# Optimization experiments

Measured on AMD Instinct MI355X. Metric: run time of the kernel, lower is better.

The kernel has to match this reference:

```python
import jax, jax.numpy as jnp
import numpy as np

T, D, H, O = 16384, 512, 1024, 512


def setup_inputs() -> dict:
    key = jax.random.key(0)
    k_in, k_h0, kU, kW, kV = jax.random.split(key, 5)
    inputs = jax.random.randint(k_in, (T,), 0, D)
    h0 = jax.random.normal(k_h0, (H,), dtype=jnp.float32)
    U = jax.random.normal(kU, (H, D), dtype=jnp.float32) * 0.01
    W = jax.random.normal(kW, (H, H), dtype=jnp.float32) * 0.01
    V = jax.random.normal(kV, (O, H), dtype=jnp.float32) * 0.01
    bh = jnp.zeros((H,), dtype=jnp.float32)
    by = jnp.zeros((O,), dtype=jnp.float32)
    return {"inputs": inputs, "h0": h0, "U": U, "W": W, "V": V, "bh": bh, "by": by}


def reference(inputs, h0, U, W, V, bh, by):
    # U @ one_hot(x_t) is just a column gather of U; precompute for all t: (T, H)
    Ux = U.T[inputs]

    def step(h, ux):
        h = jnp.tanh(ux + W @ h + bh)  # (H,)
        return h, h

    h_T, hs = jax.lax.scan(step, h0, Ux)  # hs: (T, H)
    logits = hs @ V.T + by  # (T, O)
    return logits, h_T
```

## Files before the change

### kernel.cpp

```cpp
#include <hip/hip_runtime.h>
#include <cstdint>


constexpr int T_STEPS = 16384;
constexpr int D_DIM   = 512;
constexpr int H_DIM   = 1024;
constexpr int O_DIM   = 512;
constexpr int NBLK    = 32;
constexpr int NTHR    = 512;

__device__ __forceinline__ float fast_tanh(float x) {
    float e = __expf(2.f * x);
    return 1.f - 2.f / (e + 1.f);
}

__device__ __forceinline__ float hsum4(const float4& v) {
    return (v.x + v.y) + (v.z + v.w);
}

__global__ __launch_bounds__(NTHR, 2)
void rnn_fused(const int* __restrict__ xs, const float* __restrict__ h0,
               const float* __restrict__ U, const float* __restrict__ W,
               const float* __restrict__ V, const float* __restrict__ bh,
               const float* __restrict__ by, float* __restrict__ out,
               unsigned long long* __restrict__ htag)
{
    const int b   = blockIdx.x;
    const int tid = threadIdx.x;
    const int w   = tid >> 6;
    const int l   = tid & 63;

    __shared__ float hl[2][H_DIM];

    const int wr0 = b * 32 + w * 4;
    float4 wreg[4][4];
#pragma unroll
    for (int j = 0; j < 4; ++j)
#pragma unroll
        for (int q = 0; q < 4; ++q)
            wreg[j][q] = *(const float4*)(W + (size_t)(wr0 + j) * H_DIM + 16 * l + 4 * q);
    const float bh_r = bh[wr0 + (l & 3)];
    const int   urow = wr0 + (l & 3);

    const int vr0 = b * 16 + w * 2;
    float4 vreg[2][4];
#pragma unroll
    for (int m = 0; m < 2; ++m)
#pragma unroll
        for (int q = 0; q < 4; ++q)
            vreg[m][q] = *(const float4*)(V + (size_t)(vr0 + m) * H_DIM + 16 * l + 4 * q);
    const float by_r = by[vr0 + (l & 1)];

    int rdw[4];
#pragma unroll
    for (int q = 0; q < 4; ++q)
        rdw[q] = 16 * l + 4 * (q ^ ((l >> 1) & 3));
    const int c   = tid >> 3;
    const int qw  = (tid >> 1) & 3;
    const int wdw = 16 * c + 4 * (qw ^ ((c >> 1) & 3)) + 2 * (tid & 1);

    const bool o1 = (l & 1) != 0, o2 = (l & 2) != 0;

    for (int t = 0; t < T_STEPS; ++t) {
        const int sb = (~t) & 1;
        float* hb = hl[sb];

        const int   xt = xs[t];
        const float uv = U[(size_t)urow * D_DIM + xt];

        float2 hpair;
        if (t == 0) {
            hpair = *(const float2*)(h0 + 2 * tid);
        } else {
            const unsigned want = (unsigned)(t - 1);
            const unsigned long long* pp = htag + (size_t)((t - 1) & 1) * H_DIM + 2 * tid;
            unsigned long long q0, q1;
            do {
                q0 = __hip_atomic_load(pp + 0, __ATOMIC_RELAXED, __HIP_MEMORY_SCOPE_AGENT);
                q1 = __hip_atomic_load(pp + 1, __ATOMIC_RELAXED, __HIP_MEMORY_SCOPE_AGENT);
            } while ((unsigned)(q0 >> 32) != want || (unsigned)(q1 >> 32) != want);
            hpair = make_float2(__uint_as_float((unsigned)q0),
                                __uint_as_float((unsigned)q1));
        }
        *(float2*)&hb[wdw] = hpair;
        __syncthreads();

        float4 h4[4];
#pragma unroll
        for (int q = 0; q < 4; ++q) h4[q] = *(const float4*)&hb[rdw[q]];

        float s[4];
#pragma unroll
        for (int j = 0; j < 4; ++j) {
            float4 a = make_float4(0.f, 0.f, 0.f, 0.f);
#pragma unroll
            for (int q = 0; q < 4; ++q) {
                a.x += wreg[j][q].x * h4[q].x;
                a.y += wreg[j][q].y * h4[q].y;
                a.z += wreg[j][q].z * h4[q].z;
                a.w += wreg[j][q].w * h4[q].w;
            }
            s[j] = hsum4(a);
        }
        float A  = o1 ? s[1] : s[0], Ax = o1 ? s[0] : s[1];
        float B  = o1 ? s[3] : s[2], Bx = o1 ? s[2] : s[3];
        A += __shfl_xor(Ax, 1);
        B += __shfl_xor(Bx, 1);
        float Cv = o2 ? B : A, Cx = o2 ? A : B;
        Cv += __shfl_xor(Cx, 2);
        Cv += __shfl_xor(Cv, 4);
        Cv += __shfl_xor(Cv, 8);
        Cv += __shfl_xor(Cv, 16);
        Cv += __shfl_xor(Cv, 32);

        const float hv = fast_tanh(Cv + bh_r + uv);
        if (l < 4) {
            const unsigned long long pk =
                ((unsigned long long)(unsigned)t << 32) | (unsigned long long)__float_as_uint(hv);
            __hip_atomic_store(htag + (size_t)(t & 1) * H_DIM + wr0 + l, pk,
                               __ATOMIC_RELAXED, __HIP_MEMORY_SCOPE_AGENT);
        }

        if (t > 0) {
            float sv[2];
#pragma unroll
            for (int m = 0; m < 2; ++m) {
                float4 a = make_float4(0.f, 0.f, 0.f, 0.f);
#pragma unroll
                for (int q = 0; q < 4; ++q) {
                    a.x += vreg[m][q].x * h4[q].x;
                    a.y += vreg[m][q].y * h4[q].y;
                    a.z += vreg[m][q].z * h4[q].z;
                    a.w += vreg[m][q].w * h4[q].w;
                }
                sv[m] = hsum4(a);
            }
            float P  = o1 ? sv[1] : sv[0], Px = o1 ? sv[0] : sv[1];
            P += __shfl_xor(Px, 1);
            P += __shfl_xor(P, 2);
            P += __shfl_xor(P, 4);
            P += __shfl_xor(P, 8);
            P += __shfl_xor(P, 16);
            P += __shfl_xor(P, 32);
            if (l < 2) out[(size_t)(t - 1) * O_DIM + vr0 + l] = P + by_r;
        }
    }

    {
        const unsigned want = (unsigned)(T_STEPS - 1);
        const unsigned long long* pp = htag + (size_t)((T_STEPS - 1) & 1) * H_DIM + 2 * tid;
        unsigned long long q0, q1;
        do {
            q0 = __hip_atomic_load(pp + 0, __ATOMIC_RELAXED, __HIP_MEMORY_SCOPE_AGENT);
            q1 = __hip_atomic_load(pp + 1, __ATOMIC_RELAXED, __HIP_MEMORY_SCOPE_AGENT);
        } while ((unsigned)(q0 >> 32) != want || (unsigned)(q1 >> 32) != want);
        float2 hpair = make_float2(__uint_as_float((unsigned)q0),
                                   __uint_as_float((unsigned)q1));
        if (b == 0)
            *(float2*)&out[(size_t)T_STEPS * O_DIM + 2 * tid] = hpair;

        float* hb = hl[1];
        *(float2*)&hb[wdw] = hpair;
        __syncthreads();
        float4 h4[4];
#pragma unroll
        for (int q = 0; q < 4; ++q) h4[q] = *(const float4*)&hb[rdw[q]];
        float sv[2];
#pragma unroll
        for (int m = 0; m < 2; ++m) {
            float4 a = make_float4(0.f, 0.f, 0.f, 0.f);
#pragma unroll
            for (int q = 0; q < 4; ++q) {
                a.x += vreg[m][q].x * h4[q].x;
                a.y += vreg[m][q].y * h4[q].y;
                a.z += vreg[m][q].z * h4[q].z;
                a.w += vreg[m][q].w * h4[q].w;
            }
            sv[m] = hsum4(a);
        }
        float P  = o1 ? sv[1] : sv[0], Px = o1 ? sv[0] : sv[1];
        P += __shfl_xor(Px, 1);
        P += __shfl_xor(P, 2);
        P += __shfl_xor(P, 4);
        P += __shfl_xor(P, 8);
        P += __shfl_xor(P, 16);
        P += __shfl_xor(P, 32);
        if (l < 2) out[(size_t)(T_STEPS - 1) * O_DIM + vr0 + l] = P + by_r;
    }
}

extern "C" void kernel_launch(void* const* d_in, const int* in_sizes, int n_in,
                              void* d_out, int out_size, void* d_ws, size_t ws_size,
                              hipStream_t stream) {
    const int*   xs = (const int*)d_in[0];
    const float* h0 = (const float*)d_in[1];
    const float* U  = (const float*)d_in[2];
    const float* W  = (const float*)d_in[3];
    const float* V  = (const float*)d_in[4];
    const float* bh = (const float*)d_in[5];
    const float* by = (const float*)d_in[6];
    float* out = (float*)d_out;

    unsigned long long* htag = (unsigned long long*)d_ws;
    hipMemsetAsync(d_ws, 0xAA, 2 * H_DIM * sizeof(unsigned long long), stream);

    rnn_fused<<<NBLK, NTHR, 0, stream>>>(xs, h0, U, W, V, bh, by, out, htag);
}
```

Measured before the change: 22.87 ms.

## Co-locate all worker blocks on one XCD and poll a fast non-atomic tag copy

The kernel now launches 256 blocks. Each block reads its XCC_ID and registers in a per-XCD counter, and the first XCD to gather 32 blocks is elected; all other blocks exit. The intent is to keep the per-step cross-block handoff of h inside one XCD's L2 rather than crossing the fabric between dies. Hidden state is published twice, to a volatile copy and an agent-scope atomic copy, and consumers mostly poll the volatile copy, falling back to the atomic one every eighth try. This relies on hardware-specific co-residency and cache behaviour, risks deadlock if fewer than 32 blocks land on any one XCD, and the volatile reads may still see stale L2 data.

```diff
diff --git a/kernel.cpp b/kernel.cpp
--- a/kernel.cpp
+++ b/kernel.cpp
@@ -6,16 +6,43 @@
 constexpr int D_DIM   = 512;
 constexpr int H_DIM   = 1024;
 constexpr int O_DIM   = 512;
-constexpr int NBLK    = 32;
+constexpr int NGRID   = 256;
+constexpr int NWORK   = 32;
 constexpr int NTHR    = 512;
 
 __device__ __forceinline__ float fast_tanh(float x) {
     float e = __expf(2.f * x);
     return 1.f - 2.f / (e + 1.f);
 }
-
 __device__ __forceinline__ float hsum4(const float4& v) {
     return (v.x + v.y) + (v.z + v.w);
+}
+
+__device__ __forceinline__ float2 acquire_pair(
+    const volatile unsigned long long* fp,
+    const unsigned long long* sp, unsigned want)
+{
+    unsigned long long a, b;
+    int k = 0;
+    for (;;) {
+        if ((k++ & 7) != 7) {
+            a = fp[0];
+            b = fp[1];
+        } else {
+            a = __hip_atomic_load(sp + 0, __ATOMIC_RELAXED, __HIP_MEMORY_SCOPE_AGENT);
+            b = __hip_atomic_load(sp + 1, __ATOMIC_RELAXED, __HIP_MEMORY_SCOPE_AGENT);
+        }
+        if ((unsigned)(a >> 32) == want && (unsigned)(b >> 32) == want) break;
+    }
+    return make_float2(__uint_as_float((unsigned)a), __uint_as_float((unsigned)b));
+}
+
+__device__ __forceinline__ void publish(volatile unsigned long long* Fd,
+                                        unsigned long long* Sd,
+                                        unsigned long long pk)
+{
+    *Fd = pk;
+    __hip_atomic_store(Sd, pk, __ATOMIC_RELAXED, __HIP_MEMORY_SCOPE_AGENT);
 }
 
 __global__ __launch_bounds__(NTHR, 2)
@@ -23,12 +50,36 @@
                const float* __restrict__ U, const float* __restrict__ W,
                const float* __restrict__ V, const float* __restrict__ bh,
                const float* __restrict__ by, float* __restrict__ out,
-               unsigned long long* __restrict__ htag)
+               int* __restrict__ ctrl,
+               unsigned long long* __restrict__ htagF,
+               unsigned long long* __restrict__ htagS)
 {
-    const int b   = blockIdx.x;
     const int tid = threadIdx.x;
-    const int w   = tid >> 6;
-    const int l   = tid & 63;
+
+    __shared__ int s_slice;
+    if (tid == 0) {
+        int xcd;
+        asm volatile("s_getreg_b32 %0, hwreg(HW_REG_XCC_ID)" : "=s"(xcd));
+        xcd &= 7;
+        const int r = __hip_atomic_fetch_add(&ctrl[1 + xcd], 1,
+                                             __ATOMIC_RELAXED, __HIP_MEMORY_SCOPE_AGENT);
+        if (r == NWORK - 1) {
+            int expected = 0;
+            __hip_atomic_compare_exchange_strong(&ctrl[0], &expected, xcd + 1,
+                __ATOMIC_RELAXED, __ATOMIC_RELAXED, __HIP_MEMORY_SCOPE_AGENT);
+        }
+        int ch;
+        do {
+            ch = __hip_atomic_load(&ctrl[0], __ATOMIC_RELAXED, __HIP_MEMORY_SCOPE_AGENT);
+        } while (ch == 0);
+        s_slice = (ch - 1 == xcd && r < NWORK) ? r : -1;
+    }
+    __syncthreads();
+    const int b = s_slice;
+    if (b < 0) return;
+
+    const int w = tid >> 6;
+    const int l = tid & 63;
 
     __shared__ float hl[2][H_DIM];
 
@@ -72,15 +123,8 @@
         if (t == 0) {
             hpair = *(const float2*)(h0 + 2 * tid);
         } else {
-            const unsigned want = (unsigned)(t - 1);
-            const unsigned long long* pp = htag + (size_t)((t - 1) & 1) * H_DIM + 2 * tid;
-            unsigned long long q0, q1;
-            do {
-                q0 = __hip_atomic_load(pp + 0, __ATOMIC_RELAXED, __HIP_MEMORY_SCOPE_AGENT);
-                q1 = __hip_atomic_load(pp + 1, __ATOMIC_RELAXED, __HIP_MEMORY_SCOPE_AGENT);
-            } while ((unsigned)(q0 >> 32) != want || (unsigned)(q1 >> 32) != want);
-            hpair = make_float2(__uint_as_float((unsigned)q0),
-                                __uint_as_float((unsigned)q1));
+            const size_t off = (size_t)((t - 1) & 1) * H_DIM + 2 * tid;
+            hpair = acquire_pair(htagF + off, htagS + off, (unsigned)(t - 1));
         }
         *(float2*)&hb[wdw] = hpair;
         __syncthreads();
@@ -117,8 +161,8 @@
         if (l < 4) {
             const unsigned long long pk =
                 ((unsigned long long)(unsigned)t << 32) | (unsigned long long)__float_as_uint(hv);
-            __hip_atomic_store(htag + (size_t)(t & 1) * H_DIM + wr0 + l, pk,
-                               __ATOMIC_RELAXED, __HIP_MEMORY_SCOPE_AGENT);
+            const size_t doff = (size_t)(t & 1) * H_DIM + wr0 + l;
+            publish(htagF + doff, htagS + doff, pk);
         }
 
         if (t > 0) {
@@ -147,15 +191,8 @@
     }
 
     {
-        const unsigned want = (unsigned)(T_STEPS - 1);
-        const unsigned long long* pp = htag + (size_t)((T_STEPS - 1) & 1) * H_DIM + 2 * tid;
-        unsigned long long q0, q1;
-        do {
-            q0 = __hip_atomic_load(pp + 0, __ATOMIC_RELAXED, __HIP_MEMORY_SCOPE_AGENT);
-            q1 = __hip_atomic_load(pp + 1, __ATOMIC_RELAXED, __HIP_MEMORY_SCOPE_AGENT);
-        } while ((unsigned)(q0 >> 32) != want || (unsigned)(q1 >> 32) != want);
-        float2 hpair = make_float2(__uint_as_float((unsigned)q0),
-                                   __uint_as_float((unsigned)q1));
+        const size_t off = (size_t)((T_STEPS - 1) & 1) * H_DIM + 2 * tid;
+        float2 hpair = acquire_pair(htagF + off, htagS + off, (unsigned)(T_STEPS - 1));
         if (b == 0)
             *(float2*)&out[(size_t)T_STEPS * O_DIM + 2 * tid] = hpair;
 
@@ -201,8 +238,14 @@
     const float* by = (const float*)d_in[6];
     float* out = (float*)d_out;
 
-    unsigned long long* htag = (unsigned long long*)d_ws;
-    hipMemsetAsync(d_ws, 0xAA, 2 * H_DIM * sizeof(unsigned long long), stream);
-
-    rnn_fused<<<NBLK, NTHR, 0, stream>>>(xs, h0, U, W, V, bh, by, out, htag);
-}
+    int* ctrl = (int*)d_ws;
+    unsigned long long* htagF = (unsigned long long*)((char*)d_ws + 256);
+    unsigned long long* htagS = htagF + 2 * H_DIM;
+
+    hipMemsetAsync(d_ws, 0, 256, stream);
+    hipMemsetAsync((char*)d_ws + 256, 0xAA,
+                   4 * H_DIM * sizeof(unsigned long long), stream);
+
+    rnn_fused<<<NGRID, NTHR, 0, stream>>>(xs, h0, U, W, V, bh, by, out,
+                                          ctrl, htagF, htagS);
+}
```

Result: slower. 26.20 ms (+14.6%).
